# Kernel optimization log

Hardware: AMD Instinct MI355X
Metric: run time of the kernel (lower is better)

## Reference

```python
import jax, jax.numpy as jnp
import numpy as np

B, T, H, C = 64, 2048, 128, 7


def _lstm_layer(xs, W_ih, W_hh, b):
    # xs: [T, B, H_in]; PyTorch gate order i, f, g, o
    Bsz = xs.shape[1]
    Hs = W_hh.shape[1]

    def step(carry, x_t):
        h, c = carry
        gates = x_t @ W_ih.T + h @ W_hh.T + b  # [B, 4H]
        i, f, g, o = jnp.split(gates, 4, axis=-1)
        c = jax.nn.sigmoid(f) * c + jax.nn.sigmoid(i) * jnp.tanh(g)
        h = jax.nn.sigmoid(o) * jnp.tanh(c)
        return (h, c), h

    init = (jnp.zeros((Bsz, Hs), xs.dtype), jnp.zeros((Bsz, Hs), xs.dtype))
    _, ys = jax.lax.scan(step, init, xs)
    return ys  # [T, B, H]


def setup_inputs() -> dict:
    key = jax.random.key(0)
    ks = jax.random.split(key, 12)
    s = 1.0 / np.sqrt(H)
    u = lambda k, shape: jax.random.uniform(k, shape, jnp.float32, -s, s)
    x = jax.random.normal(ks[0], (B, T, 1), jnp.float32)
    lengths = jax.random.randint(ks[1], (B,), 1, T + 1, jnp.int32)
    return {
        "x": x,
        "lengths": lengths,
        "ff_w": u(ks[2], (H, 1)),
        "ff_b": u(ks[3], (H,)),
        "W_ih0": u(ks[4], (4 * H, H)),
        "W_hh0": u(ks[5], (4 * H, H)),
        "b0": u(ks[6], (4 * H,)),  # b_ih + b_hh fused
        "W_ih1": u(ks[7], (4 * H, H)),
        "W_hh1": u(ks[8], (4 * H, H)),
        "b1": u(ks[9], (4 * H,)),
        "lin_w": u(ks[10], (C, 3 * H)),
        "lin_b": u(ks[11], (C,)),
    }


def reference(x, lengths, ff_w, ff_b, W_ih0, W_hh0, b0, W_ih1, W_hh1, b1, lin_w, lin_b):
    # input projection (Linear(1, H))
    xf = x @ ff_w.T + ff_b  # [B, T, H]
    xs = jnp.transpose(xf, (1, 0, 2))  # [T, B, H]
    h1 = _lstm_layer(xs, W_ih0, W_hh0, b0)
    h2 = _lstm_layer(h1, W_ih1, W_hh1, b1)
    out = jnp.transpose(h2, (1, 0, 2))  # [B, T, H]

    # masked mean / max / last pooling over valid timesteps
    mask = jnp.arange(T)[None, :] < lengths[:, None]  # [B, T]
    mf = mask[:, :, None].astype(out.dtype)
    mean = (out * mf).sum(axis=1) / lengths[:, None].astype(out.dtype)
    mx = jnp.max(jnp.where(mask[:, :, None], out, -jnp.inf), axis=1)
    idx = jnp.broadcast_to((lengths - 1)[:, None, None], (out.shape[0], 1, out.shape[2]))
    last = jnp.take_along_axis(out, idx, axis=1)[:, 0]
    h = jnp.concatenate([mean, mx, last], axis=-1)  # [B, 3H]
    return h @ lin_w.T + lin_b  # [B, C]
```

## Files before the change

kernel.cpp:

```cpp
#include <hip/hip_runtime.h>
#include <hip/hip_fp16.h>

#define TT 2048
#define BB 64
#define HH 128
#define GG 512
#define CH 64
#define NCH (TT / CH)

typedef _Float16 f16x8 __attribute__((ext_vector_type(8)));
typedef _Float16 f16x4 __attribute__((ext_vector_type(4)));
typedef float f32x4 __attribute__((ext_vector_type(4)));

__device__ __forceinline__ float sigm(float x) {
    return __builtin_amdgcn_rcpf(1.0f + __expf(-x));
}
__device__ __forceinline__ float tanh_f(float x) {
    return 1.0f - 2.0f * __builtin_amdgcn_rcpf(1.0f + __expf(2.0f * x));
}
__device__ __forceinline__ void bar_lds() {
    asm volatile("s_waitcnt lgkmcnt(0)\n\ts_barrier" ::: "memory");
}

__device__ __forceinline__ f16x8 load_frag(const float* rowp, int kt, int lh) {
    const float4* p4 = (const float4*)(rowp + kt * 32 + lh * 8);
    float4 a = p4[0], b = p4[1];
    f16x8 f;
    f[0] = (_Float16)a.x; f[1] = (_Float16)a.y; f[2] = (_Float16)a.z; f[3] = (_Float16)a.w;
    f[4] = (_Float16)b.x; f[5] = (_Float16)b.y; f[6] = (_Float16)b.z; f[7] = (_Float16)b.w;
    return f;
}

__global__ __launch_bounds__(512, 1) void k_pipe(
    const float* __restrict__ x, const int* __restrict__ lengths,
    const float* __restrict__ ff_w, const float* __restrict__ ff_b,
    const float* __restrict__ W_ih0, const float* __restrict__ W_hh0,
    const float* __restrict__ b0, const float* __restrict__ W_ih1,
    const float* __restrict__ W_hh1, const float* __restrict__ b1,
    _Float16* __restrict__ h0g, int* __restrict__ flags,
    float* __restrict__ pooled) {
    const int tid = threadIdx.x;
    const int w = tid >> 6;
    const int lane = tid & 63;
    const int c = lane & 15;
    const int lh = lane >> 4;
    const int un = 16 * w + c;
    const bool ard = (c == 0);
    const bool wr16 = (lane < 16);

    __shared__ float xs[TT];
    __shared__ _Float16 Hb0[2][HH];
    __shared__ _Float16 Hb1[2][HH];
    __shared__ _Float16 Qs[CH][GG];

    if (blockIdx.x < BB) {
        const int b = blockIdx.x;
        for (int i = tid; i < TT; i += 512) xs[i] = x[b * TT + i];
        if (tid < 2 * HH) ((_Float16*)Hb0)[tid] = (_Float16)0.f;

        f16x8 Bf[4][4];
        float v[4], u0[4];
#pragma unroll
        for (int t2 = 0; t2 < 4; ++t2) {
            const int r = t2 * HH + un;
#pragma unroll
            for (int kt = 0; kt < 4; ++kt) Bf[t2][kt] = load_frag(W_hh0 + r * HH, kt, lh);
            const float4* wi4 = (const float4*)(W_ih0 + r * HH);
            const float4* fw4 = (const float4*)ff_w;
            const float4* fb4 = (const float4*)ff_b;
            float vv = 0.f, uu = 0.f;
#pragma unroll
            for (int m = 0; m < HH / 4; ++m) {
                float4 a = wi4[m], fw = fw4[m], fb = fb4[m];
                vv += a.x * fw.x + a.y * fw.y + a.z * fw.z + a.w * fw.w;
                uu += a.x * fb.x + a.y * fb.y + a.z * fb.z + a.w * fb.w;
            }
            v[t2] = vv;
            u0[t2] = uu + b0[r];
        }
#pragma unroll
        for (int t2 = 0; t2 < 4; ++t2)
#pragma unroll
            for (int kt = 0; kt < 4; ++kt) asm volatile("" : "+v"(Bf[t2][kt]));

        float cst0 = 0.f;
        f16x8 av[4];
        f32x4 accLo[4], accHi[4];
#pragma unroll
        for (int kt = 0; kt < 4; ++kt) {
            av[kt] = (f16x8){0, 0, 0, 0, 0, 0, 0, 0};
            accLo[kt] = (f32x4){0.f, 0.f, 0.f, 0.f};
            accHi[kt] = (f32x4){0.f, 0.f, 0.f, 0.f};
        }
        __syncthreads();

#define PSTEP(T_, RB_, XT_)                                                     \
    do {                                                                        \
        if (ard) {                                                              \
            _Pragma("unroll") for (int kt = 0; kt < 4; ++kt)                    \
                av[kt] = *(const f16x8*)&Hb0[RB_][kt * 32 + lh * 8];            \
        }                                                                       \
        float p[4];                                                             \
        _Pragma("unroll") for (int t2 = 0; t2 < 4; ++t2) {                      \
            const float ci = (XT_) * v[t2] + u0[t2];                            \
            accLo[t2][0] = ci;                                                  \
            accHi[t2][0] = 0.f;                                                 \
            accLo[t2] = __builtin_amdgcn_mfma_f32_16x16x32_f16(av[0], Bf[t2][0],\
                                                               accLo[t2], 0, 0, 0);\
            accHi[t2] = __builtin_amdgcn_mfma_f32_16x16x32_f16(av[2], Bf[t2][2],\
                                                               accHi[t2], 0, 0, 0);\
            accLo[t2] = __builtin_amdgcn_mfma_f32_16x16x32_f16(av[1], Bf[t2][1],\
                                                               accLo[t2], 0, 0, 0);\
            accHi[t2] = __builtin_amdgcn_mfma_f32_16x16x32_f16(av[3], Bf[t2][3],\
                                                               accHi[t2], 0, 0, 0);\
            p[t2] = accLo[t2][0] + accHi[t2][0];                                \
        }                                                                       \
        float gi = sigm(p[0]), gf = sigm(p[1]);                                 \
        float gg = tanh_f(p[2]), go = sigm(p[3]);                               \
        cst0 = gf * cst0 + gi * gg;                                             \
        float h0n = go * tanh_f(cst0);                                          \
        if (wr16) {                                                             \
            Hb0[(RB_) ^ 1][un] = (_Float16)h0n;                                 \
            __builtin_nontemporal_store(                                        \
                (_Float16)h0n, h0g + ((size_t)b * TT + (T_)) * HH + un);        \
        }                                                                       \
        bar_lds();                                                              \
    } while (0)

        for (int ch = 0; ch < NCH; ++ch) {
            const int t0 = ch * CH;
            for (int j = 0; j < CH; j += 2) {
                const float xt0 = xs[t0 + j];
                const float xt1 = xs[t0 + j + 1];
                PSTEP(t0 + j, 0, xt0);
                PSTEP(t0 + j + 1, 1, xt1);
            }
            __syncthreads();
            if (tid == 0)
                __hip_atomic_store(&flags[b * NCH + ch], ch + 1, __ATOMIC_RELEASE,
                                   __HIP_MEMORY_SCOPE_AGENT);
        }
#undef PSTEP
    } else {
        const int b = blockIdx.x - BB;
        if (tid < 2 * HH) ((_Float16*)Hb1)[tid] = (_Float16)0.f;

        f16x8 Bh[4][4];
        float bb1[4];
#pragma unroll
        for (int t2 = 0; t2 < 4; ++t2) {
#pragma unroll
            for (int kt = 0; kt < 4; ++kt)
                Bh[t2][kt] = load_frag(W_hh1 + (t2 * HH + un) * HH, kt, lh);
            bb1[t2] = b1[t2 * HH + un];
        }
#pragma unroll
        for (int t2 = 0; t2 < 4; ++t2)
#pragma unroll
            for (int kt = 0; kt < 4; ++kt) asm volatile("" : "+v"(Bh[t2][kt]));

        const int len = lengths[b];
        float cst1 = 0.f, mean = 0.f, mx = -1e30f, last = 0.f;
        f16x8 av[4];
#pragma unroll
        for (int kt = 0; kt < 4; ++kt) av[kt] = (f16x8){0, 0, 0, 0, 0, 0, 0, 0};
        __syncthreads();

#define CSTEP(T_, RB_, QV_)                                                     \
    do {                                                                        \
        if (ard) {                                                              \
            _Pragma("unroll") for (int kt = 0; kt < 4; ++kt)                    \
                av[kt] = *(const f16x8*)&Hb1[RB_][kt * 32 + lh * 8];            \
        }                                                                       \
        float p[4];                                                             \
        _Pragma("unroll") for (int t2 = 0; t2 < 4; ++t2) {                      \
            accLo[t2][0] = (float)(QV_)[t2];                                    \
            accHi[t2][0] = 0.f;                                                 \
            accLo[t2] = __builtin_amdgcn_mfma_f32_16x16x32_f16(av[0], Bh[t2][0],\
                                                               accLo[t2], 0, 0, 0);\
            accHi[t2] = __builtin_amdgcn_mfma_f32_16x16x32_f16(av[2], Bh[t2][2],\
                                                               accHi[t2], 0, 0, 0);\
            accLo[t2] = __builtin_amdgcn_mfma_f32_16x16x32_f16(av[1], Bh[t2][1],\
                                                               accLo[t2], 0, 0, 0);\
            accHi[t2] = __builtin_amdgcn_mfma_f32_16x16x32_f16(av[3], Bh[t2][3],\
                                                               accHi[t2], 0, 0, 0);\
            p[t2] = accLo[t2][0] + accHi[t2][0];                                \
        }                                                                       \
        float gi = sigm(p[0]), gf = sigm(p[1]);                                 \
        float gg = tanh_f(p[2]), go = sigm(p[3]);                               \
        cst1 = gf * cst1 + gi * gg;                                             \
        float h1n = go * tanh_f(cst1);                                          \
        if (wr16) Hb1[(RB_) ^ 1][un] = (_Float16)h1n;                           \
        if ((T_) < len) {                                                       \
            mean += h1n;                                                        \
            mx = fmaxf(mx, h1n);                                                \
        }                                                                       \
        if ((T_) == len - 1) last = h1n;                                        \
        bar_lds();                                                              \
    } while (0)

        for (int ch = 0; ch < NCH; ++ch) {
            if (tid == 0) {
                int guard = 0;
                while (__hip_atomic_load(&flags[b * NCH + ch], __ATOMIC_ACQUIRE,
                                         __HIP_MEMORY_SCOPE_AGENT) != ch + 1) {
                    __builtin_amdgcn_s_sleep(8);
                    if (++guard > (1 << 22)) break;
                }
            }
            __syncthreads();
            f16x8 Bi[4][4];
#pragma unroll
            for (int t2 = 0; t2 < 4; ++t2)
#pragma unroll
                for (int kt = 0; kt < 4; ++kt)
                    Bi[t2][kt] = load_frag(W_ih1 + (t2 * HH + un) * HH, kt, lh);
            const _Float16* hbase = h0g + ((size_t)b * TT + ch * CH) * HH;
#pragma unroll
            for (int mt = 0; mt < 4; ++mt) {
                f16x8 am[4];
#pragma unroll
                for (int kt = 0; kt < 4; ++kt)
                    am[kt] = *(const f16x8*)(hbase + (mt * 16 + c) * HH + kt * 32 + lh * 8);
                f32x4 qa[4];
#pragma unroll
                for (int t2 = 0; t2 < 4; ++t2) {
                    qa[t2] = (f32x4){0.f, 0.f, 0.f, 0.f};
#pragma unroll
                    for (int kt = 0; kt < 4; ++kt)
                        qa[t2] = __builtin_amdgcn_mfma_f32_16x16x32_f16(
                            am[kt], Bi[t2][kt], qa[t2], 0, 0, 0);
                }
#pragma unroll
                for (int r = 0; r < 4; ++r) {
                    f16x4 qv;
#pragma unroll
                    for (int t2 = 0; t2 < 4; ++t2) qv[t2] = (_Float16)(qa[t2][r] + bb1[t2]);
                    *(f16x4*)&Qs[mt * 16 + 4 * lh + r][un * 4] = qv;
                }
            }
            __syncthreads();
            f32x4 accLo[4], accHi[4];
#pragma unroll
            for (int t2 = 0; t2 < 4; ++t2) {
                accLo[t2] = (f32x4){0.f, 0.f, 0.f, 0.f};
                accHi[t2] = (f32x4){0.f, 0.f, 0.f, 0.f};
            }
            const int t0 = ch * CH;
            for (int j = 0; j < CH; j += 2) {
                const f16x4 qv0 = *(const f16x4*)&Qs[j][un * 4];
                const f16x4 qv1 = *(const f16x4*)&Qs[j + 1][un * 4];
                CSTEP(t0 + j, 0, qv0);
                CSTEP(t0 + j + 1, 1, qv1);
            }
        }
#undef CSTEP
        if (wr16) {
            pooled[b * 384 + un] = mean / (float)len;
            pooled[b * 384 + 128 + un] = mx;
            pooled[b * 384 + 256 + un] = last;
        }
    }
}

__global__ __launch_bounds__(448) void k_head(
    const float* __restrict__ pooled, const float* __restrict__ lin_w,
    const float* __restrict__ lin_b, float* __restrict__ out) {
    int tid = threadIdx.x;
    int b = tid / 7, cc = tid % 7;
    const float* p = pooled + b * 384;
    const float* wr = lin_w + cc * 384;
    float a0 = 0.f, a1 = 0.f, a2 = 0.f, a3 = 0.f;
#pragma unroll
    for (int k = 0; k < 384; k += 4) {
        a0 += p[k + 0] * wr[k + 0];
        a1 += p[k + 1] * wr[k + 1];
        a2 += p[k + 2] * wr[k + 2];
        a3 += p[k + 3] * wr[k + 3];
    }
    out[tid] = lin_b[cc] + ((a0 + a1) + (a2 + a3));
}

extern "C" void kernel_launch(void* const* d_in, const int* in_sizes, int n_in,
                              void* d_out, int out_size, void* d_ws, size_t ws_size,
                              hipStream_t stream) {
    const float* x     = (const float*)d_in[0];
    const int*   lens  = (const int*)d_in[1];
    const float* ff_w  = (const float*)d_in[2];
    const float* ff_b  = (const float*)d_in[3];
    const float* W_ih0 = (const float*)d_in[4];
    const float* W_hh0 = (const float*)d_in[5];
    const float* b0    = (const float*)d_in[6];
    const float* W_ih1 = (const float*)d_in[7];
    const float* W_hh1 = (const float*)d_in[8];
    const float* b1    = (const float*)d_in[9];
    const float* lin_w = (const float*)d_in[10];
    const float* lin_b = (const float*)d_in[11];
    float* out = (float*)d_out;

    char* ws = (char*)d_ws;
    const size_t HBYTES = (size_t)BB * TT * HH * 2;
    _Float16* h0g = (_Float16*)ws;
    int* flags    = (int*)(ws + HBYTES);
    float* pooled = (float*)(ws + HBYTES + 8192);

    k_pipe<<<dim3(2 * BB), dim3(512), 0, stream>>>(
        x, lens, ff_w, ff_b, W_ih0, W_hh0, b0, W_ih1, W_hh1, b1, h0g, flags, pooled);
    k_head<<<dim3(1), dim3(448), 0, stream>>>(pooled, lin_w, lin_b, out);
}
```

Before: 1.395 ms.

## Replace per-step MFMA recurrence with 4-lane fdot2 dot products and shuffles

Both recurrent layers drop the per-timestep MFMA matvec, of which only one output row was used. Each of 4 lanes per hidden unit now holds a quarter of that unit's four gate rows in registers. Partial sums are formed with packed fp16 fdot2 and combined with two xor shuffles, then one lane applies the gate nonlinearities and writes h. The goal is to shorten the serial per-step latency and use every lane. The cost is more VALU work per step and repacking of fp16 pairs into fdot2 operands.

```diff
diff --git a/kernel.cpp b/kernel.cpp
--- a/kernel.cpp
+++ b/kernel.cpp
@@ -10,6 +10,7 @@
 
 typedef _Float16 f16x8 __attribute__((ext_vector_type(8)));
 typedef _Float16 f16x4 __attribute__((ext_vector_type(4)));
+typedef _Float16 f16x2 __attribute__((ext_vector_type(2)));
 typedef float f32x4 __attribute__((ext_vector_type(4)));
 
 __device__ __forceinline__ float sigm(float x) {
@@ -29,6 +30,22 @@
     f[0] = (_Float16)a.x; f[1] = (_Float16)a.y; f[2] = (_Float16)a.z; f[3] = (_Float16)a.w;
     f[4] = (_Float16)b.x; f[5] = (_Float16)b.y; f[6] = (_Float16)b.z; f[7] = (_Float16)b.w;
     return f;
+}
+
+__device__ __forceinline__ float dot_q(const f16x8* Wg, const f16x8* hq) {
+    float a = 0.f, b = 0.f;
+#pragma unroll
+    for (int j = 0; j < 2; ++j)
+#pragma unroll
+        for (int d = 0; d < 4; ++d) {
+            a = __builtin_amdgcn_fdot2(
+                (f16x2){Wg[j][2 * d], Wg[j][2 * d + 1]},
+                (f16x2){hq[j][2 * d], hq[j][2 * d + 1]}, a, false);
+            b = __builtin_amdgcn_fdot2(
+                (f16x2){Wg[2 + j][2 * d], Wg[2 + j][2 * d + 1]},
+                (f16x2){hq[2 + j][2 * d], hq[2 + j][2 * d + 1]}, b, false);
+        }
+    return a + b;
 }
 
 __global__ __launch_bounds__(512, 1) void k_pipe(
@@ -45,8 +62,9 @@
     const int c = lane & 15;
     const int lh = lane >> 4;
     const int un = 16 * w + c;
-    const bool ard = (c == 0);
-    const bool wr16 = (lane < 16);
+    const int n = tid >> 2;
+    const int q = tid & 3;
+    const bool q0 = (q == 0);
 
     __shared__ float xs[TT];
     __shared__ _Float16 Hb0[2][HH];
@@ -58,13 +76,13 @@
         for (int i = tid; i < TT; i += 512) xs[i] = x[b * TT + i];
         if (tid < 2 * HH) ((_Float16*)Hb0)[tid] = (_Float16)0.f;
 
-        f16x8 Bf[4][4];
-        float v[4], u0[4];
-#pragma unroll
-        for (int t2 = 0; t2 < 4; ++t2) {
-            const int r = t2 * HH + un;
-#pragma unroll
-            for (int kt = 0; kt < 4; ++kt) Bf[t2][kt] = load_frag(W_hh0 + r * HH, kt, lh);
+        f16x8 Wr[4][4];
+        float v4[4], u4[4];
+#pragma unroll
+        for (int g = 0; g < 4; ++g) {
+            const int r = g * HH + n;
+#pragma unroll
+            for (int j = 0; j < 4; ++j) Wr[g][j] = load_frag(W_hh0 + r * HH, q, j);
             const float4* wi4 = (const float4*)(W_ih0 + r * HH);
             const float4* fw4 = (const float4*)ff_w;
             const float4* fb4 = (const float4*)ff_b;
@@ -75,54 +93,40 @@
                 vv += a.x * fw.x + a.y * fw.y + a.z * fw.z + a.w * fw.w;
                 uu += a.x * fb.x + a.y * fb.y + a.z * fb.z + a.w * fb.w;
             }
-            v[t2] = vv;
-            u0[t2] = uu + b0[r];
-        }
-#pragma unroll
-        for (int t2 = 0; t2 < 4; ++t2)
-#pragma unroll
-            for (int kt = 0; kt < 4; ++kt) asm volatile("" : "+v"(Bf[t2][kt]));
+            v4[g] = vv;
+            u4[g] = uu + b0[r];
+        }
+#pragma unroll
+        for (int g = 0; g < 4; ++g)
+#pragma unroll
+            for (int j = 0; j < 4; ++j) asm volatile("" : "+v"(Wr[g][j]));
 
         float cst0 = 0.f;
-        f16x8 av[4];
-        f32x4 accLo[4], accHi[4];
-#pragma unroll
-        for (int kt = 0; kt < 4; ++kt) {
-            av[kt] = (f16x8){0, 0, 0, 0, 0, 0, 0, 0};
-            accLo[kt] = (f32x4){0.f, 0.f, 0.f, 0.f};
-            accHi[kt] = (f32x4){0.f, 0.f, 0.f, 0.f};
-        }
         __syncthreads();
 
 #define PSTEP(T_, RB_, XT_)                                                     \
     do {                                                                        \
-        if (ard) {                                                              \
-            _Pragma("unroll") for (int kt = 0; kt < 4; ++kt)                    \
-                av[kt] = *(const f16x8*)&Hb0[RB_][kt * 32 + lh * 8];            \
+        f16x8 hq[4];                                                            \
+        _Pragma("unroll") for (int j = 0; j < 4; ++j)                           \
+            hq[j] = *(const f16x8*)&Hb0[RB_][32 * q + 8 * j];                   \
+        float p[4];                                                             \
+        _Pragma("unroll") for (int g = 0; g < 4; ++g) p[g] = dot_q(Wr[g], hq);  \
+        _Pragma("unroll") for (int g = 0; g < 4; ++g) {                         \
+            p[g] += __shfl_xor(p[g], 1, 4);                                     \
+            p[g] += __shfl_xor(p[g], 2, 4);                                     \
         }                                                                       \
-        float p[4];                                                             \
-        _Pragma("unroll") for (int t2 = 0; t2 < 4; ++t2) {                      \
-            const float ci = (XT_) * v[t2] + u0[t2];                            \
-            accLo[t2][0] = ci;                                                  \
-            accHi[t2][0] = 0.f;                                                 \
-            accLo[t2] = __builtin_amdgcn_mfma_f32_16x16x32_f16(av[0], Bf[t2][0],\
-                                                               accLo[t2], 0, 0, 0);\
-            accHi[t2] = __builtin_amdgcn_mfma_f32_16x16x32_f16(av[2], Bf[t2][2],\
-                                                               accHi[t2], 0, 0, 0);\
-            accLo[t2] = __builtin_amdgcn_mfma_f32_16x16x32_f16(av[1], Bf[t2][1],\
-                                                               accLo[t2], 0, 0, 0);\
-            accHi[t2] = __builtin_amdgcn_mfma_f32_16x16x32_f16(av[3], Bf[t2][3],\
-                                                               accHi[t2], 0, 0, 0);\
-            p[t2] = accLo[t2][0] + accHi[t2][0];                                \
-        }                                                                       \
-        float gi = sigm(p[0]), gf = sigm(p[1]);                                 \
-        float gg = tanh_f(p[2]), go = sigm(p[3]);                               \
-        cst0 = gf * cst0 + gi * gg;                                             \
-        float h0n = go * tanh_f(cst0);                                          \
-        if (wr16) {                                                             \
-            Hb0[(RB_) ^ 1][un] = (_Float16)h0n;                                 \
+        if (q0) {                                                               \
+            float s0 = p[0] + (XT_) * v4[0] + u4[0];                            \
+            float s1 = p[1] + (XT_) * v4[1] + u4[1];                            \
+            float s2 = p[2] + (XT_) * v4[2] + u4[2];                            \
+            float s3 = p[3] + (XT_) * v4[3] + u4[3];                            \
+            float gi = sigm(s0), gf = sigm(s1);                                 \
+            float gg = tanh_f(s2), go = sigm(s3);                               \
+            cst0 = gf * cst0 + gi * gg;                                         \
+            float h0n = go * tanh_f(cst0);                                      \
+            Hb0[(RB_) ^ 1][n] = (_Float16)h0n;                                  \
             __builtin_nontemporal_store(                                        \
-                (_Float16)h0n, h0g + ((size_t)b * TT + (T_)) * HH + un);        \
+                (_Float16)h0n, h0g + ((size_t)b * TT + (T_)) * HH + n);         \
         }                                                                       \
         bar_lds();                                                              \
     } while (0)
@@ -145,57 +149,51 @@
         const int b = blockIdx.x - BB;
         if (tid < 2 * HH) ((_Float16*)Hb1)[tid] = (_Float16)0.f;
 
-        f16x8 Bh[4][4];
+        f16x8 Wr[4][4];
         float bb1[4];
 #pragma unroll
-        for (int t2 = 0; t2 < 4; ++t2) {
-#pragma unroll
-            for (int kt = 0; kt < 4; ++kt)
-                Bh[t2][kt] = load_frag(W_hh1 + (t2 * HH + un) * HH, kt, lh);
-            bb1[t2] = b1[t2 * HH + un];
-        }
-#pragma unroll
-        for (int t2 = 0; t2 < 4; ++t2)
-#pragma unroll
-            for (int kt = 0; kt < 4; ++kt) asm volatile("" : "+v"(Bh[t2][kt]));
+        for (int g = 0; g < 4; ++g) {
+            const int r = g * HH + n;
+#pragma unroll
+            for (int j = 0; j < 4; ++j) Wr[g][j] = load_frag(W_hh1 + r * HH, q, j);
+            bb1[g] = b1[g * HH + un];
+        }
+#pragma unroll
+        for (int g = 0; g < 4; ++g)
+#pragma unroll
+            for (int j = 0; j < 4; ++j) asm volatile("" : "+v"(Wr[g][j]));
 
         const int len = lengths[b];
         float cst1 = 0.f, mean = 0.f, mx = -1e30f, last = 0.f;
-        f16x8 av[4];
-#pragma unroll
-        for (int kt = 0; kt < 4; ++kt) av[kt] = (f16x8){0, 0, 0, 0, 0, 0, 0, 0};
         __syncthreads();
 
 #define CSTEP(T_, RB_, QV_)                                                     \
     do {                                                                        \
-        if (ard) {                                                              \
-            _Pragma("unroll") for (int kt = 0; kt < 4; ++kt)                    \
-                av[kt] = *(const f16x8*)&Hb1[RB_][kt * 32 + lh * 8];            \
+        f16x8 hq[4];                                                            \
+        _Pragma("unroll") for (int j = 0; j < 4; ++j)                           \
+            hq[j] = *(const f16x8*)&Hb1[RB_][32 * q + 8 * j];                   \
+        float p[4];                                                             \
+        _Pragma("unroll") for (int g = 0; g < 4; ++g) p[g] = dot_q(Wr[g], hq);  \
+        _Pragma("unroll") for (int g = 0; g < 4; ++g) {                         \
+            p[g] += __shfl_xor(p[g], 1, 4);                                     \
+            p[g] += __shfl_xor(p[g], 2, 4);                                     \
         }                                                                       \
-        float p[4];                                                             \
-        _Pragma("unroll") for (int t2 = 0; t2 < 4; ++t2) {                      \
-            accLo[t2][0] = (float)(QV_)[t2];                                    \
-            accHi[t2][0] = 0.f;                                                 \
-            accLo[t2] = __builtin_amdgcn_mfma_f32_16x16x32_f16(av[0], Bh[t2][0],\
-                                                               accLo[t2], 0, 0, 0);\
-            accHi[t2] = __builtin_amdgcn_mfma_f32_16x16x32_f16(av[2], Bh[t2][2],\
-                                                               accHi[t2], 0, 0, 0);\
-            accLo[t2] = __builtin_amdgcn_mfma_f32_16x16x32_f16(av[1], Bh[t2][1],\
-                                                               accLo[t2], 0, 0, 0);\
-            accHi[t2] = __builtin_amdgcn_mfma_f32_16x16x32_f16(av[3], Bh[t2][3],\
-                                                               accHi[t2], 0, 0, 0);\
-            p[t2] = accLo[t2][0] + accHi[t2][0];                                \
+        if (q0) {                                                               \
+            float s0 = p[0] + (float)(QV_)[0];                                  \
+            float s1 = p[1] + (float)(QV_)[1];                                  \
+            float s2 = p[2] + (float)(QV_)[2];                                  \
+            float s3 = p[3] + (float)(QV_)[3];                                  \
+            float gi = sigm(s0), gf = sigm(s1);                                 \
+            float gg = tanh_f(s2), go = sigm(s3);                               \
+            cst1 = gf * cst1 + gi * gg;                                         \
+            float h1n = go * tanh_f(cst1);                                      \
+            Hb1[(RB_) ^ 1][n] = (_Float16)h1n;                                  \
+            if ((T_) < len) {                                                   \
+                mean += h1n;                                                    \
+                mx = fmaxf(mx, h1n);                                            \
+            }                                                                   \
+            if ((T_) == len - 1) last = h1n;                                    \
         }                                                                       \
-        float gi = sigm(p[0]), gf = sigm(p[1]);                                 \
-        float gg = tanh_f(p[2]), go = sigm(p[3]);                               \
-        cst1 = gf * cst1 + gi * gg;                                             \
-        float h1n = go * tanh_f(cst1);                                          \
-        if (wr16) Hb1[(RB_) ^ 1][un] = (_Float16)h1n;                           \
-        if ((T_) < len) {                                                       \
-            mean += h1n;                                                        \
-            mx = fmaxf(mx, h1n);                                                \
-        }                                                                       \
-        if ((T_) == len - 1) last = h1n;                                        \
         bar_lds();                                                              \
     } while (0)
 
@@ -240,25 +238,19 @@
                 }
             }
             __syncthreads();
-            f32x4 accLo[4], accHi[4];
-#pragma unroll
-            for (int t2 = 0; t2 < 4; ++t2) {
-                accLo[t2] = (f32x4){0.f, 0.f, 0.f, 0.f};
-                accHi[t2] = (f32x4){0.f, 0.f, 0.f, 0.f};
-            }
             const int t0 = ch * CH;
             for (int j = 0; j < CH; j += 2) {
-                const f16x4 qv0 = *(const f16x4*)&Qs[j][un * 4];
-                const f16x4 qv1 = *(const f16x4*)&Qs[j + 1][un * 4];
+                const f16x4 qv0 = *(const f16x4*)&Qs[j][n * 4];
+                const f16x4 qv1 = *(const f16x4*)&Qs[j + 1][n * 4];
                 CSTEP(t0 + j, 0, qv0);
                 CSTEP(t0 + j + 1, 1, qv1);
             }
         }
 #undef CSTEP
-        if (wr16) {
-            pooled[b * 384 + un] = mean / (float)len;
-            pooled[b * 384 + 128 + un] = mx;
-            pooled[b * 384 + 256 + un] = last;
+        if (q0) {
+            pooled[b * 384 + n] = mean / (float)len;
+            pooled[b * 384 + 128 + n] = mx;
+            pooled[b * 384 + 256 + n] = last;
         }
     }
 }
```

After: 1.745 ms. 1.25x slower.
